# Kernel optimization log

Hardware: AMD Instinct MI355X
Metric: run time of the kernel (lower is better)

The kernel has to match this reference:

```python
import jax, jax.numpy as jnp
import numpy as np

LN_EPS = 1e-5


def setup_inputs() -> dict:
    key = jax.random.key(0)
    ks = jax.random.split(key, 4)
    B, L, Dm, N = 16, 2048, 512, 64
    return {
        "x": jax.random.normal(ks[0], (B, L, Dm), dtype=jnp.float32),
        "A": jax.random.normal(ks[1], (Dm, N), dtype=jnp.float32),
        "C": jax.random.normal(ks[2], (Dm, N), dtype=jnp.float32),
        "D": jax.random.normal(ks[3], (Dm,), dtype=jnp.float32),
        "gamma": jnp.ones((Dm,), dtype=jnp.float32),
        "beta": jnp.zeros((Dm,), dtype=jnp.float32),
    }


def reference(x, A, C, D, gamma, beta):
    # LayerNorm over last dim (matches nn.LayerNorm(d_model))
    mean = jnp.mean(x, axis=-1, keepdims=True)
    var = jnp.mean(jnp.square(x - mean), axis=-1, keepdims=True)
    x_norm = (x - mean) * jax.lax.rsqrt(var + LN_EPS) * gamma + beta

    B, L, Dm = x.shape
    N = A.shape[1]
    h0 = jnp.zeros((B, N), dtype=x.dtype)

    def step(h, u):
        # u: [B, Dm]; h: [B, N]
        h = jnp.tanh(u @ A + h)
        y = h @ C.T + u * D  # [B, Dm]
        return h, y

    # scan over time: xs [L, B, Dm]
    _, ys = jax.lax.scan(step, h0, jnp.swapaxes(x_norm, 0, 1))
    out = jnp.swapaxes(ys, 0, 1)  # [B, L, Dm]
    return out + x
```

## Files before the change

### kernel.cpp

```cpp
#include <hip/hip_runtime.h>
#include <hip/hip_bf16.h>

typedef short bf16x8 __attribute__((ext_vector_type(8)));
typedef float f32x4 __attribute__((ext_vector_type(4)));

constexpr int B_ = 16;
constexpr int L_ = 2048;
constexpr int DM = 512;
constexpr int NS = 64;
constexpr int BL = B_ * L_;
constexpr float LN_EPS = 1e-5f;
constexpr float KLN = 2.8853900817779268f;

constexpr int SEGS = 32;
constexpr int LSEG = L_ / SEGS;
constexpr int WARM = 64;

__device__ __forceinline__ unsigned f32bits(float f) {
    union { float f; unsigned u; } v{f}; return v.u;
}
__device__ __forceinline__ float bitsf32(unsigned u) {
    union { unsigned u; float f; } v{u}; return v.f;
}
__device__ __forceinline__ unsigned short f2bf(float f) {
    unsigned u = f32bits(f);
    unsigned r = u + 0x7FFF + ((u >> 16) & 1);
    return (unsigned short)(r >> 16);
}

__device__ __forceinline__ void norm_split8(float4 u0, float4 u1,
                                            float rstd, float m2,
                                            bf16x8& ah, bf16x8& al) {
    float t[8] = { fmaf(u0.x, rstd, m2), fmaf(u0.y, rstd, m2),
                   fmaf(u0.z, rstd, m2), fmaf(u0.w, rstd, m2),
                   fmaf(u1.x, rstd, m2), fmaf(u1.y, rstd, m2),
                   fmaf(u1.z, rstd, m2), fmaf(u1.w, rstd, m2) };
    unsigned hb[8], lb[8];
    #pragma unroll
    for (int j = 0; j < 8; ++j) {
        unsigned tb = f32bits(t[j]);
        hb[j] = tb & 0xFFFF0000u;
        lb[j] = f32bits(t[j] - bitsf32(hb[j]));
    }
    union { unsigned u[4]; bf16x8 v; } H, L;
    #pragma unroll
    for (int p = 0; p < 4; ++p) {
        H.u[p] = (hb[2*p] >> 16) | hb[2*p+1];
        L.u[p] = (lb[2*p] >> 16) | (lb[2*p+1] & 0xFFFF0000u);
    }
    ah = H.v; al = L.v;
}

__global__ __launch_bounds__(256) void k_pack(const float* __restrict__ A,
                                              const float* __restrict__ C,
                                              const float* __restrict__ gamma,
                                              const float* __restrict__ beta,
                                              const float* __restrict__ Dv,
                                              unsigned short* __restrict__ PAh,
                                              unsigned short* __restrict__ PAl,
                                              unsigned short* __restrict__ PC,
                                              float* __restrict__ c0,
                                              float* __restrict__ gd,
                                              float* __restrict__ bd) {
    const int blk = blockIdx.x;
    const int tid = threadIdx.x;
    if (blk < 32) {
        const int g = blk * 256 + tid;
        if (g < 4096) {
            const int lane = g & 63, ct = (g >> 6) & 3, k32 = (g >> 8) & 3, kc = g >> 10;
            const int kbase = kc * 128 + k32 * 32 + (lane >> 4) * 8;
            const int col   = ct * 16 + (lane & 15);
            unsigned hb[8], lb[8];
            #pragma unroll
            for (int j = 0; j < 8; ++j) {
                float v = gamma[kbase + j] * A[(size_t)(kbase + j) * NS + col];
                unsigned tb = f32bits(v);
                hb[j] = tb & 0xFFFF0000u;
                lb[j] = f32bits(v - bitsf32(hb[j]));
            }
            uint4 ph, pl;
            ph.x = (hb[0] >> 16) | hb[1]; ph.y = (hb[2] >> 16) | hb[3];
            ph.z = (hb[4] >> 16) | hb[5]; ph.w = (hb[6] >> 16) | hb[7];
            pl.x = (lb[0] >> 16) | (lb[1] & 0xFFFF0000u);
            pl.y = (lb[2] >> 16) | (lb[3] & 0xFFFF0000u);
            pl.z = (lb[4] >> 16) | (lb[5] & 0xFFFF0000u);
            pl.w = (lb[6] >> 16) | (lb[7] & 0xFFFF0000u);
            *reinterpret_cast<uint4*>(PAh + (size_t)g * 8) = ph;
            *reinterpret_cast<uint4*>(PAl + (size_t)g * 8) = pl;
        } else {
            const int g2 = g - 4096;
            unsigned short v[8];
            #pragma unroll
            for (int j = 0; j < 8; ++j) v[j] = f2bf(C[(size_t)g2 * 8 + j]);
            uint4 p;
            p.x = v[0] | ((unsigned)v[1] << 16); p.y = v[2] | ((unsigned)v[3] << 16);
            p.z = v[4] | ((unsigned)v[5] << 16); p.w = v[6] | ((unsigned)v[7] << 16);
            *reinterpret_cast<uint4*>(PC + (size_t)g2 * 8) = p;
        }
    } else {
        __shared__ float red[256];
        #pragma unroll
        for (int i = 0; i < 2; ++i) {
            int d = tid + 256 * i;
            gd[d] = gamma[d] * Dv[d];
            bd[d] = beta[d] * Dv[d];
        }
        const int n = tid & 63, part = tid >> 6;
        float s = 0.f;
        #pragma unroll 8
        for (int k = part * 128; k < part * 128 + 128; ++k)
            s += beta[k] * A[(size_t)k * NS + n];
        red[tid] = s;
        __syncthreads();
        if (tid < 64)
            c0[tid] = red[tid] + red[tid + 64] + red[tid + 128] + red[tid + 192];
    }
}

__global__ __launch_bounds__(256) void k_gemmA(const float* __restrict__ x,
                                               const unsigned short* __restrict__ PAh,
                                               const unsigned short* __restrict__ PAl,
                                               const float* __restrict__ c0,
                                               float* __restrict__ stats,
                                               float* __restrict__ Bu) {
    const int tid  = threadIdx.x;
    const int r0   = blockIdx.x * 64;
    const int w    = tid >> 6;
    const int lane = tid & 63;
    const int myrow = 16 * w + (lane & 15);
    const int kb    = (lane >> 4) * 8;
    const float* xrow = x + (size_t)(r0 + myrow) * DM;

    float s = 0.f, s2 = 0.f;
    #pragma unroll
    for (int kc = 0; kc < 4; ++kc) {
        #pragma unroll
        for (int k32 = 0; k32 < 4; ++k32) {
            float4 a = *reinterpret_cast<const float4*>(xrow + kc * 128 + k32 * 32 + kb);
            float4 b = *reinterpret_cast<const float4*>(xrow + kc * 128 + k32 * 32 + kb + 4);
            s  += (a.x + a.y) + (a.z + a.w) + (b.x + b.y) + (b.z + b.w);
            s2 += a.x*a.x + a.y*a.y + a.z*a.z + a.w*a.w
                + b.x*b.x + b.y*b.y + b.z*b.z + b.w*b.w;
        }
    }
    s += __shfl_xor(s, 16); s2 += __shfl_xor(s2, 16);
    s += __shfl_xor(s, 32); s2 += __shfl_xor(s2, 32);
    const float mean = s * (1.0f / DM);
    const float var  = s2 * (1.0f / DM) - mean * mean;
    const float rstd = rsqrtf(var + LN_EPS);
    const float m2   = -mean * rstd;
    if (lane < 16) {
        stats[2 * (r0 + myrow)]     = mean;
        stats[2 * (r0 + myrow) + 1] = rstd;
    }

    f32x4 acc[4] = {};
    const bf16x8* ABh = reinterpret_cast<const bf16x8*>(PAh);
    const bf16x8* ABl = reinterpret_cast<const bf16x8*>(PAl);
    #pragma unroll
    for (int kc = 0; kc < 4; ++kc) {
        #pragma unroll
        for (int k32 = 0; k32 < 4; ++k32) {
            float4 u0 = *reinterpret_cast<const float4*>(xrow + kc * 128 + k32 * 32 + kb);
            float4 u1 = *reinterpret_cast<const float4*>(xrow + kc * 128 + k32 * 32 + kb + 4);
            bf16x8 ah, al;
            norm_split8(u0, u1, rstd, m2, ah, al);
            #pragma unroll
            for (int ct = 0; ct < 4; ++ct) {
                const int fi = ((kc * 4 + k32) * 4 + ct) * 64 + lane;
                bf16x8 bh = ABh[fi];
                bf16x8 bl = ABl[fi];
                acc[ct] = __builtin_amdgcn_mfma_f32_16x16x32_bf16(ah, bh, acc[ct], 0, 0, 0);
                acc[ct] = __builtin_amdgcn_mfma_f32_16x16x32_bf16(ah, bl, acc[ct], 0, 0, 0);
                acc[ct] = __builtin_amdgcn_mfma_f32_16x16x32_bf16(al, bh, acc[ct], 0, 0, 0);
            }
        }
    }

    const int orow = r0 + 16 * w + (lane >> 4) * 4;
    #pragma unroll
    for (int ct = 0; ct < 4; ++ct) {
        const int n = ct * 16 + (lane & 15);
        const float c0n = c0[n];
        #pragma unroll
        for (int j = 0; j < 4; ++j)
            Bu[(size_t)(orow + j) * NS + n] = acc[ct][j] + c0n;
    }
}

__global__ __launch_bounds__(512, 4) void k_scanC(const float* __restrict__ x,
                                                  const unsigned short* __restrict__ PC,
                                                  const float* __restrict__ gd,
                                                  const float* __restrict__ bd,
                                                  const float* __restrict__ stats,
                                                  const float* __restrict__ Bu,
                                                  float* __restrict__ out) {
    __shared__ unsigned short Hs[64 * 64];
    const int tid = threadIdx.x;
    const int seg = blockIdx.x & (SEGS - 1);
    const int b   = blockIdx.x >> 5;
    const int l0  = seg * LSEG;
    const int rowbase = b * L_ + l0;

    if (tid < 64) {
        constexpr int G = 16;
        const int n     = tid;
        const int start = (seg == 0) ? 0 : (l0 - WARM);
        const int skip  = l0 - start;
        const int nGrp  = (l0 + LSEG - start) / G;
        const float* bp = Bu + ((size_t)b * L_ + start) * NS + n;
        char* hbase = reinterpret_cast<char*>(Hs);

        float bufA[G], bufB[G];
        #pragma unroll
        for (int j = 0; j < G; ++j) bufA[j] = KLN * bp[(size_t)j * NS];
        float hv = 0.0f;
        int g = 0;
        for (;;) {
            {
                if (g + 1 < nGrp) {
                    const int base = (g + 1) * G;
                    #pragma unroll
                    for (int j = 0; j < G; ++j)
                        bufB[j] = KLN * bp[(size_t)(base + j) * NS];
                }
                const int lbase = g * G - skip;
                const bool doStore = lbase >= 0;
                #pragma unroll
                for (int j = 0; j < G; ++j) {
                    float t = fmaf(hv, KLN, bufA[j]);
                    float e = __builtin_amdgcn_exp2f(t);
                    float rr = __builtin_amdgcn_rcpf(e + 1.0f);
                    hv = fmaf(-2.0f, rr, 1.0f);
                    if (doStore) {
                        const int lr = lbase + j;
                        *reinterpret_cast<unsigned short*>(
                            hbase + lr * 128 + ((2 * n) ^ ((lr & 7) << 4))) = f2bf(hv);
                    }
                }
            }
            if (++g == nGrp) break;
            {
                if (g + 1 < nGrp) {
                    const int base = (g + 1) * G;
                    #pragma unroll
                    for (int j = 0; j < G; ++j)
                        bufA[j] = KLN * bp[(size_t)(base + j) * NS];
                }
                const int lbase = g * G - skip;
                const bool doStore = lbase >= 0;
                #pragma unroll
                for (int j = 0; j < G; ++j) {
                    float t = fmaf(hv, KLN, bufB[j]);
                    float e = __builtin_amdgcn_exp2f(t);
                    float rr = __builtin_amdgcn_rcpf(e + 1.0f);
                    hv = fmaf(-2.0f, rr, 1.0f);
                    if (doStore) {
                        const int lr = lbase + j;
                        *reinterpret_cast<unsigned short*>(
                            hbase + lr * 128 + ((2 * n) ^ ((lr & 7) << 4))) = f2bf(hv);
                    }
                }
            }
            if (++g == nGrp) break;
        }
    }
    __syncthreads();

    const int w    = tid >> 6;
    const int lane = tid & 63;
    const int rt   = w >> 1;
    const int dh   = (w & 1) * 256;
    const int arow = rt * 16 + (lane & 15);

    bf16x8 afr[2];
    #pragma unroll
    for (int kt = 0; kt < 2; ++kt) {
        const int byte = arow * 128 + ((kt * 64 + (lane >> 4) * 16) ^ ((arow & 7) << 4));
        afr[kt] = *reinterpret_cast<const bf16x8*>(
            reinterpret_cast<const char*>(Hs) + byte);
    }

    const int rb = rowbase + rt * 16 + (lane >> 4) * 4;
    float mean_[4], rstd_[4];
    #pragma unroll
    for (int j = 0; j < 4; ++j) {
        mean_[j] = stats[2 * (rb + j)];
        rstd_[j] = stats[2 * (rb + j) + 1];
    }

    const int dl = dh + (lane & 15);
    const int n0 = (lane >> 4) * 8;
    #pragma unroll
    for (int ct = 0; ct < 16; ++ct) {
        const int d = dl + ct * 16;
        bf16x8 b0 = *reinterpret_cast<const bf16x8*>(PC + (size_t)d * NS + n0);
        bf16x8 b1 = *reinterpret_cast<const bf16x8*>(PC + (size_t)d * NS + 32 + n0);
        f32x4 a = {};
        a = __builtin_amdgcn_mfma_f32_16x16x32_bf16(afr[0], b0, a, 0, 0, 0);
        a = __builtin_amdgcn_mfma_f32_16x16x32_bf16(afr[1], b1, a, 0, 0, 0);
        const float gdv = gd[d];
        const float bdv = bd[d];
        #pragma unroll
        for (int j = 0; j < 4; ++j) {
            const size_t idx = (size_t)(rb + j) * DM + d;
            const float xv = x[idx];
            const float z  = (xv - mean_[j]) * rstd_[j];
            out[idx] = a[j] + z * gdv + bdv + xv;
        }
    }
}

extern "C" void kernel_launch(void* const* d_in, const int* in_sizes, int n_in,
                              void* d_out, int out_size, void* d_ws, size_t ws_size,
                              hipStream_t stream) {
    const float* x     = (const float*)d_in[0];
    const float* A     = (const float*)d_in[1];
    const float* C     = (const float*)d_in[2];
    const float* Dv    = (const float*)d_in[3];
    const float* gamma = (const float*)d_in[4];
    const float* beta  = (const float*)d_in[5];
    float* out = (float*)d_out;

    char* ws = (char*)d_ws;
    float* Bu           = (float*)(ws);
    float* stats        = (float*)(ws + (size_t)BL * NS * 4);
    char* p = ws + (size_t)BL * NS * 4 + (size_t)BL * 2 * 4;
    unsigned short* PAh = (unsigned short*)p;        p += (size_t)DM * NS * 2;
    unsigned short* PAl = (unsigned short*)p;        p += (size_t)DM * NS * 2;
    unsigned short* PC  = (unsigned short*)p;        p += (size_t)DM * NS * 2;
    float* c0           = (float*)p;                 p += 256;
    float* gd           = (float*)p;                 p += (size_t)DM * 4;
    float* bd           = (float*)p;

    k_pack<<<33, 256, 0, stream>>>(A, C, gamma, beta, Dv, PAh, PAl, PC, c0, gd, bd);
    k_gemmA<<<BL / 64, 256, 0, stream>>>(x, PAh, PAl, c0, stats, Bu);
    k_scanC<<<B_ * SEGS, 512, 0, stream>>>(x, PC, gd, bd, stats, Bu, out);
}
```

Measured before the change: 73.06 us.

## Transpose C-projection MFMA so each lane writes contiguous float4 output rows

```diff
diff --git a/kernel.cpp b/kernel.cpp
--- a/kernel.cpp
+++ b/kernel.cpp
@@ -58,7 +58,7 @@
                                               const float* __restrict__ Dv,
                                               unsigned short* __restrict__ PAh,
                                               unsigned short* __restrict__ PAl,
-                                              unsigned short* __restrict__ PC,
+                                              unsigned short* __restrict__ PC2,
                                               float* __restrict__ c0,
                                               float* __restrict__ gd,
                                               float* __restrict__ bd) {
@@ -88,14 +88,21 @@
             *reinterpret_cast<uint4*>(PAh + (size_t)g * 8) = ph;
             *reinterpret_cast<uint4*>(PAl + (size_t)g * 8) = pl;
         } else {
-            const int g2 = g - 4096;
+            const int g2   = g - 4096;
+            const int lane = g2 & 63;
+            const int kt   = (g2 >> 6) & 1;
+            const int offs = (g2 >> 7) & 1;
+            const int dblk = g2 >> 8;
+            const int i    = lane & 15;
+            const int d    = dblk * 32 + ((i >> 2) * 8) + offs * 4 + (i & 3);
+            const int nb   = kt * 32 + (lane >> 4) * 8;
             unsigned short v[8];
             #pragma unroll
-            for (int j = 0; j < 8; ++j) v[j] = f2bf(C[(size_t)g2 * 8 + j]);
+            for (int j = 0; j < 8; ++j) v[j] = f2bf(C[(size_t)d * NS + nb + j]);
             uint4 p;
             p.x = v[0] | ((unsigned)v[1] << 16); p.y = v[2] | ((unsigned)v[3] << 16);
             p.z = v[4] | ((unsigned)v[5] << 16); p.w = v[6] | ((unsigned)v[7] << 16);
-            *reinterpret_cast<uint4*>(PC + (size_t)g2 * 8) = p;
+            *reinterpret_cast<uint4*>(PC2 + (size_t)g2 * 8) = p;
         }
     } else {
         __shared__ float red[256];
@@ -189,13 +196,13 @@
 }
 
 __global__ __launch_bounds__(512, 4) void k_scanC(const float* __restrict__ x,
-                                                  const unsigned short* __restrict__ PC,
+                                                  const unsigned short* __restrict__ PC2,
                                                   const float* __restrict__ gd,
                                                   const float* __restrict__ bd,
                                                   const float* __restrict__ stats,
                                                   const float* __restrict__ Bu,
                                                   float* __restrict__ out) {
-    __shared__ unsigned short Hs[64 * 64];
+    __shared__ __align__(16) char smem[8192 + 4096];
     const int tid = threadIdx.x;
     const int seg = blockIdx.x & (SEGS - 1);
     const int b   = blockIdx.x >> 5;
@@ -209,7 +216,7 @@
         const int skip  = l0 - start;
         const int nGrp  = (l0 + LSEG - start) / G;
         const float* bp = Bu + ((size_t)b * L_ + start) * NS + n;
-        char* hbase = reinterpret_cast<char*>(Hs);
+        char* hbase = smem;
 
         float bufA[G], bufB[G];
         #pragma unroll
@@ -264,50 +271,67 @@
             }
             if (++g == nGrp) break;
         }
+    } else {
+        float* GdS = (float*)(smem + 8192);
+        const int t2 = tid - 64;
+        if (t2 < 256)
+            reinterpret_cast<float4*>(GdS)[t2] =
+                (t2 < 128) ? reinterpret_cast<const float4*>(gd)[t2]
+                           : reinterpret_cast<const float4*>(bd)[t2 - 128];
     }
     __syncthreads();
 
     const int w    = tid >> 6;
     const int lane = tid & 63;
-    const int rt   = w >> 1;
-    const int dh   = (w & 1) * 256;
-    const int arow = rt * 16 + (lane & 15);
-
-    bf16x8 afr[2];
-    #pragma unroll
-    for (int kt = 0; kt < 2; ++kt) {
-        const int byte = arow * 128 + ((kt * 64 + (lane >> 4) * 16) ^ ((arow & 7) << 4));
-        afr[kt] = *reinterpret_cast<const bf16x8*>(
-            reinterpret_cast<const char*>(Hs) + byte);
-    }
-
-    const int rb = rowbase + rt * 16 + (lane >> 4) * 4;
-    float mean_[4], rstd_[4];
-    #pragma unroll
-    for (int j = 0; j < 4; ++j) {
-        mean_[j] = stats[2 * (rb + j)];
-        rstd_[j] = stats[2 * (rb + j) + 1];
-    }
-
-    const int dl = dh + (lane & 15);
-    const int n0 = (lane >> 4) * 8;
-    #pragma unroll
-    for (int ct = 0; ct < 16; ++ct) {
-        const int d = dl + ct * 16;
-        bf16x8 b0 = *reinterpret_cast<const bf16x8*>(PC + (size_t)d * NS + n0);
-        bf16x8 b1 = *reinterpret_cast<const bf16x8*>(PC + (size_t)d * NS + 32 + n0);
-        f32x4 a = {};
-        a = __builtin_amdgcn_mfma_f32_16x16x32_bf16(afr[0], b0, a, 0, 0, 0);
-        a = __builtin_amdgcn_mfma_f32_16x16x32_bf16(afr[1], b1, a, 0, 0, 0);
-        const float gdv = gd[d];
-        const float bdv = bd[d];
-        #pragma unroll
-        for (int j = 0; j < 4; ++j) {
-            const size_t idx = (size_t)(rb + j) * DM + d;
-            const float xv = x[idx];
-            const float z  = (xv - mean_[j]) * rstd_[j];
-            out[idx] = a[j] + z * gdv + bdv + xv;
-        }
+    const int rg   = w & 3;
+    const int half = w >> 2;
+    const int hr   = rg * 16 + (lane & 15);
+    const int kb   = (lane >> 4) * 8;
+    const int grow = rowbase + hr;
+    const float mean = stats[2 * grow];
+    const float rstd = stats[2 * grow + 1];
+
+    bf16x8 hfr0 = *reinterpret_cast<const bf16x8*>(
+        smem + hr * 128 + (((lane >> 4) * 16) ^ ((hr & 7) << 4)));
+    bf16x8 hfr1 = *reinterpret_cast<const bf16x8*>(
+        smem + hr * 128 + ((64 + (lane >> 4) * 16) ^ ((hr & 7) << 4)));
+
+    const float* GdS = (const float*)(smem + 8192);
+    const float* BdS = GdS + DM;
+    const float* xrp = x + (size_t)grow * DM;
+    float* orp = out + (size_t)grow * DM;
+
+    #pragma unroll
+    for (int i = 0; i < 8; ++i) {
+        const int dblk = half * 8 + i;
+        bf16x8 c00 = *reinterpret_cast<const bf16x8*>(PC2 + ((size_t)dblk * 256 + lane) * 8);
+        bf16x8 c01 = *reinterpret_cast<const bf16x8*>(PC2 + ((size_t)dblk * 256 + 64 + lane) * 8);
+        bf16x8 c10 = *reinterpret_cast<const bf16x8*>(PC2 + ((size_t)dblk * 256 + 128 + lane) * 8);
+        bf16x8 c11 = *reinterpret_cast<const bf16x8*>(PC2 + ((size_t)dblk * 256 + 192 + lane) * 8);
+        f32x4 a0 = {}, a1 = {};
+        a0 = __builtin_amdgcn_mfma_f32_16x16x32_bf16(c00, hfr0, a0, 0, 0, 0);
+        a0 = __builtin_amdgcn_mfma_f32_16x16x32_bf16(c01, hfr1, a0, 0, 0, 0);
+        a1 = __builtin_amdgcn_mfma_f32_16x16x32_bf16(c10, hfr0, a1, 0, 0, 0);
+        a1 = __builtin_amdgcn_mfma_f32_16x16x32_bf16(c11, hfr1, a1, 0, 0, 0);
+
+        const int db = dblk * 32 + kb;
+        const float4 x0 = *reinterpret_cast<const float4*>(xrp + db);
+        const float4 x1 = *reinterpret_cast<const float4*>(xrp + db + 4);
+        const float4 g0 = *reinterpret_cast<const float4*>(GdS + db);
+        const float4 g1 = *reinterpret_cast<const float4*>(GdS + db + 4);
+        const float4 d0 = *reinterpret_cast<const float4*>(BdS + db);
+        const float4 d1 = *reinterpret_cast<const float4*>(BdS + db + 4);
+        float4 o0, o1;
+        o0.x = fmaf((x0.x - mean) * rstd, g0.x, a0[0] + d0.x + x0.x);
+        o0.y = fmaf((x0.y - mean) * rstd, g0.y, a0[1] + d0.y + x0.y);
+        o0.z = fmaf((x0.z - mean) * rstd, g0.z, a0[2] + d0.z + x0.z);
+        o0.w = fmaf((x0.w - mean) * rstd, g0.w, a0[3] + d0.w + x0.w);
+        o1.x = fmaf((x1.x - mean) * rstd, g1.x, a1[0] + d1.x + x1.x);
+        o1.y = fmaf((x1.y - mean) * rstd, g1.y, a1[1] + d1.y + x1.y);
+        o1.z = fmaf((x1.z - mean) * rstd, g1.z, a1[2] + d1.z + x1.z);
+        o1.w = fmaf((x1.w - mean) * rstd, g1.w, a1[3] + d1.w + x1.w);
+        *reinterpret_cast<float4*>(orp + db)     = o0;
+        *reinterpret_cast<float4*>(orp + db + 4) = o1;
     }
 }
 
@@ -328,12 +352,12 @@
     char* p = ws + (size_t)BL * NS * 4 + (size_t)BL * 2 * 4;
     unsigned short* PAh = (unsigned short*)p;        p += (size_t)DM * NS * 2;
     unsigned short* PAl = (unsigned short*)p;        p += (size_t)DM * NS * 2;
-    unsigned short* PC  = (unsigned short*)p;        p += (size_t)DM * NS * 2;
+    unsigned short* PC2 = (unsigned short*)p;        p += (size_t)DM * NS * 2;
     float* c0           = (float*)p;                 p += 256;
     float* gd           = (float*)p;                 p += (size_t)DM * 4;
     float* bd           = (float*)p;
 
-    k_pack<<<33, 256, 0, stream>>>(A, C, gamma, beta, Dv, PAh, PAl, PC, c0, gd, bd);
+    k_pack<<<33, 256, 0, stream>>>(A, C, gamma, beta, Dv, PAh, PAl, PC2, c0, gd, bd);
     k_gemmA<<<BL / 64, 256, 0, stream>>>(x, PAh, PAl, c0, stats, Bu);
-    k_scanC<<<B_ * SEGS, 512, 0, stream>>>(x, PC, gd, bd, stats, Bu, out);
-}
+    k_scanC<<<B_ * SEGS, 512, 0, stream>>>(x, PC2, gd, bd, stats, Bu, out);
+}
```

New measurement: 68.93 us, median of 2. -5.7%, faster.
